# Optimization experiments

Hardware: AMD Instinct MI355X
Metric: run time of the kernel (lower is better)

The kernel has to match this reference:

```python
import jax, jax.numpy as jnp
import numpy as np

N = 131072   # total nodes (4096 molecules x ~32 atoms)
E = 524288   # directed edges (avg degree 4)
G = 4096     # number of graphs
D_IN, D_H, D_OUT = 128, 512, 256
BN_EPS = 1e-5


def setup_inputs() -> dict:
    key = jax.random.key(0)
    ks = jax.random.split(key, 24)
    def rn(i, shape, s=0.05):
        return jax.random.normal(ks[i], shape, jnp.float32) * s
    inp = {
        "x": jax.random.normal(ks[0], (N, D_IN), jnp.float32),
        "edge_index": jax.random.randint(ks[1], (2, E), 0, N),
        "batch": jnp.sort(jax.random.randint(ks[2], (N,), 0, G)),
        # GCN layer weights (stored [in, out]) and biases
        "W1": rn(3, (D_IN, D_H)), "b1": jnp.zeros((D_H,), jnp.float32),
        "W2": rn(4, (D_H, D_H)),  "b2": jnp.zeros((D_H,), jnp.float32),
        "W3": rn(5, (D_H, D_OUT)), "b3": jnp.zeros((D_OUT,), jnp.float32),
        # BatchNorm (eval mode): gamma, beta, running_mean, running_var
        "g1": jnp.ones((D_H,), jnp.float32),  "be1": jnp.zeros((D_H,), jnp.float32),
        "m1": rn(6, (D_H,)),  "v1": jax.random.uniform(ks[7], (D_H,), jnp.float32) + 0.5,
        "g2": jnp.ones((D_H,), jnp.float32),  "be2": jnp.zeros((D_H,), jnp.float32),
        "m2": rn(8, (D_H,)),  "v2": jax.random.uniform(ks[9], (D_H,), jnp.float32) + 0.5,
        "g3": jnp.ones((D_OUT,), jnp.float32), "be3": jnp.zeros((D_OUT,), jnp.float32),
        "m3": rn(10, (D_OUT,)), "v3": jax.random.uniform(ks[11], (D_OUT,), jnp.float32) + 0.5,
        # MLP head
        "Wf1": rn(12, (D_OUT, D_OUT)), "bf1": jnp.zeros((D_OUT,), jnp.float32),
        "Wf2": rn(13, (D_OUT, D_OUT)), "bf2": jnp.zeros((D_OUT,), jnp.float32),
    }
    return inp


def reference(x, edge_index, batch, W1, b1, W2, b2, W3, b3,
              g1, be1, m1, v1, g2, be2, m2, v2, g3, be3, m3, v3,
              Wf1, bf1, Wf2, bf2):
    loop = jnp.arange(N)
    src = jnp.concatenate([edge_index[0], loop])  # add self-loops (PyG GCNConv default)
    dst = jnp.concatenate([edge_index[1], loop])
    deg = jax.ops.segment_sum(jnp.ones((E + N,), x.dtype), dst, num_segments=N)
    dinv = jnp.where(deg > 0, jax.lax.rsqrt(deg), 0.0)
    norm = dinv[src] * dinv[dst]                  # D^{-1/2} A_hat D^{-1/2}

    def gcn(h, W, b):
        h = h @ W                                 # dense GEMM [N, d_out]
        msg = h[src] * norm[:, None]              # gather + scale
        return jax.ops.segment_sum(msg, dst, num_segments=N) + b  # scatter-add

    def bn(h, g, be, m, v):                       # eval-mode BatchNorm1d
        return g * (h - m) * jax.lax.rsqrt(v + BN_EPS) + be

    h = bn(jax.nn.relu(gcn(x, W1, b1)), g1, be1, m1, v1)
    h = bn(jax.nn.relu(gcn(h, W2, b2)), g2, be2, m2, v2)
    h = bn(jax.nn.relu(gcn(h, W3, b3)), g3, be3, m3, v3)

    sums = jax.ops.segment_sum(h, batch, num_segments=G)          # global_mean_pool
    cnt = jax.ops.segment_sum(jnp.ones((N,), h.dtype), batch, num_segments=G)
    pooled = sums / jnp.maximum(cnt, 1.0)[:, None]

    return jax.nn.relu(pooled @ Wf1 + bf1) @ Wf2 + bf2
```

## Files before the change

kernel.cpp:

```cpp
#include <hip/hip_runtime.h>

static constexpr int NN = 131072;
static constexpr int NE = 524288;
static constexpr int NG = 4096;

typedef __attribute__((ext_vector_type(8))) short short8;
typedef __attribute__((ext_vector_type(4))) float f32x4;
typedef __attribute__((ext_vector_type(2))) float f32x2;

__device__ __forceinline__ float bfbits2f(unsigned b) {
    return __uint_as_float(b << 16);
}
__device__ __forceinline__ unsigned short f2bfbits(float f) {
    unsigned u = __float_as_uint(f);
    u += 0x7fffu + ((u >> 16) & 1u);
    return (unsigned short)(u >> 16);
}
__device__ __forceinline__ unsigned pack2(float a, float b) {
    return (unsigned)f2bfbits(a) | ((unsigned)f2bfbits(b) << 16);
}

__device__ __forceinline__ int geti(const void* p, size_t i, int w64) {
    return w64 ? (int)((const long long*)p)[i] : ((const int*)p)[i];
}

#if __has_builtin(__builtin_amdgcn_cvt_pk_f32_fp8) && __has_builtin(__builtin_amdgcn_cvt_pk_fp8_f32)
#define FP8_CVT_HW 1
#else
#define FP8_CVT_HW 0
#endif

__device__ __forceinline__ float e4m32f(unsigned b) {
    unsigned e = (b >> 3) & 0xFu, m = b & 7u;
    float v = e ? __uint_as_float(((e + 120u) << 23) | (m << 20))
                : (float)m * 0.001953125f;
    return (b & 0x80u) ? -v : v;
}
__device__ __forceinline__ unsigned f2e4m3(float f) {
    unsigned u = __float_as_uint(f);
    unsigned s = (u >> 24) & 0x80u;
    unsigned mag = u & 0x7fffffffu;
    if (mag >= 0x43e00000u) return s | 0x7eu;
    if (mag < 0x3c800000u) {
        int q = (int)(__uint_as_float(mag) * 512.0f + 0.5f);
        return s | (unsigned)q;
    }
    unsigned r = mag + 0x0007ffffu + ((mag >> 20) & 1u);
    if (r >= 0x43e00000u) return s | 0x7eu;
    return s | (((r >> 23) - 120u) << 3) | ((r >> 20) & 7u);
}

template<bool HI>
__device__ __forceinline__ unsigned dec_pair(unsigned w) {
#if FP8_CVT_HW
    f32x2 p = __builtin_amdgcn_cvt_pk_f32_fp8((int)w, HI);
    return __builtin_amdgcn_perm(__float_as_uint(p.y), __float_as_uint(p.x), 0x07060302u);
#else
    unsigned b0 = HI ? ((w >> 16) & 255u) : (w & 255u);
    unsigned b1 = HI ? (w >> 24) : ((w >> 8) & 255u);
    return pack2(e4m32f(b0), e4m32f(b1));
#endif
}

__device__ __forceinline__ short8 dec8(uint2 u) {
    union { uint4 q; short8 s; } r;
    r.q.x = dec_pair<false>(u.x);
    r.q.y = dec_pair<true>(u.x);
    r.q.z = dec_pair<false>(u.y);
    r.q.w = dec_pair<true>(u.y);
    return r.s;
}

__device__ __forceinline__ void dec4f(unsigned w, float* v) {
#if FP8_CVT_HW
    f32x2 a = __builtin_amdgcn_cvt_pk_f32_fp8((int)w, false);
    f32x2 b = __builtin_amdgcn_cvt_pk_f32_fp8((int)w, true);
    v[0] = a.x; v[1] = a.y; v[2] = b.x; v[3] = b.y;
#else
#pragma unroll
    for (int i = 0; i < 4; ++i) v[i] = e4m32f((w >> (8 * i)) & 0xffu);
#endif
}

__device__ __forceinline__ unsigned enc4(float a, float b, float c, float d) {
#if FP8_CVT_HW
    int r = __builtin_amdgcn_cvt_pk_fp8_f32(a, b, 0, false);
    r = __builtin_amdgcn_cvt_pk_fp8_f32(c, d, r, true);
    return (unsigned)r;
#else
    return f2e4m3(a) | (f2e4m3(b) << 8) | (f2e4m3(c) << 16) | (f2e4m3(d) << 24);
#endif
}
__device__ __forceinline__ unsigned enc1(float a) {
#if FP8_CVT_HW
    return (unsigned)__builtin_amdgcn_cvt_pk_fp8_f32(a, a, 0, false) & 0xffu;
#else
    return f2e4m3(a);
#endif
}

__device__ __forceinline__ void gld16(const void* g, void* l, int lane) {
#if __has_builtin(__builtin_amdgcn_global_load_lds)
    __builtin_amdgcn_global_load_lds((const __attribute__((address_space(1))) unsigned int*)g,
                                     (__attribute__((address_space(3))) unsigned int*)l, 16, 0, 0);
#else
    *(uint4*)((char*)l + lane * 16) = *(const uint4*)g;
#endif
}

__global__ void k_detect(const void* __restrict__ eidx, const void* __restrict__ batch,
                         int* __restrict__ flags) {
    const int* e32 = (const int*)eidx;
    const int* b32 = (const int*)batch;
    int e64 = (e32[1] == 0 && e32[2001] == 0 && e32[40001] == 0 && e32[2 * NE - 1] == 0) ? 1 : 0;
    int b64 = (b32[NN - 1] == 0) ? 1 : 0;
    flags[0] = e64;
    flags[1] = b64;
}


__global__ void k_zero(int* __restrict__ p, int n) {
    int i = blockIdx.x * 256 + threadIdx.x;
    if (i < n) p[i] = 0;
}

__global__ void k_transpose(const float* __restrict__ W,
                            unsigned short* __restrict__ Wt, int K, int Ncols) {
    int idx = blockIdx.x * 256 + threadIdx.x;
    if (idx >= K * Ncols) return;
    int k = idx / Ncols, n = idx - k * Ncols;
    Wt[n * K + k] = f2bfbits(W[idx]);
}

__global__ void k_bn_prep(const float* __restrict__ g, const float* __restrict__ be,
                          const float* __restrict__ m, const float* __restrict__ v,
                          float* __restrict__ s, float* __restrict__ t, int d) {
    int i = blockIdx.x * 256 + threadIdx.x;
    if (i >= d) return;
    float inv = rsqrtf(v[i] + 1e-5f);
    float sc = g[i] * inv;
    s[i] = sc;
    t[i] = be[i] - m[i] * sc;
}

__global__ void k_deg_count(const void* __restrict__ eidx, const int* __restrict__ flags,
                            int* __restrict__ cnt) {
    int i = blockIdx.x * 256 + threadIdx.x;
    if (i >= NE) return;
    int d = geti(eidx, (size_t)NE + i, flags[0]);
    atomicAdd(&cnt[d], 1);
}

__global__ __launch_bounds__(1024) void k_scan(const int* __restrict__ cnt, int* __restrict__ rowptr,
                                               float* __restrict__ dinv) {
    __shared__ int part[1024];
    const int t = threadIdx.x;
    const int base = t * 128;
    const int4* c4 = (const int4*)(cnt + base);
    int s = 0;
#pragma unroll
    for (int i = 0; i < 32; ++i) { int4 u = c4[i]; s += u.x + u.y + u.z + u.w; }
    part[t] = s;
    __syncthreads();
    for (int off = 1; off < 1024; off <<= 1) {
        int v = (t >= off) ? part[t - off] : 0;
        __syncthreads();
        part[t] += v;
        __syncthreads();
    }
    int ex = (t == 0) ? 0 : part[t - 1];
#pragma unroll
    for (int i = 0; i < 32; ++i) {
        int4 u = c4[i];
        int4 o; o.x = ex; o.y = ex + u.x; o.z = o.y + u.y; o.w = o.z + u.z; ex = o.w + u.w;
        *(int4*)(rowptr + base + 4 * i) = o;
        float4 dv;
        dv.x = rsqrtf((float)(u.x + 1)); dv.y = rsqrtf((float)(u.y + 1));
        dv.z = rsqrtf((float)(u.z + 1)); dv.w = rsqrtf((float)(u.w + 1));
        *(float4*)(dinv + base + 4 * i) = dv;
    }
    if (t == 1023) rowptr[NN] = ex;
}

__global__ void k_fill(const void* __restrict__ eidx, const int* __restrict__ flags,
                       const int* __restrict__ rowptr, int* __restrict__ fillp,
                       int* __restrict__ col) {
    int i = blockIdx.x * 256 + threadIdx.x;
    if (i >= NE) return;
    int e64 = flags[0];
    int s = geti(eidx, (size_t)i, e64);
    int d = geti(eidx, (size_t)NE + i, e64);
    int p = rowptr[d] + atomicAdd(&fillp[d], 1);
    col[p] = s;
}

__global__ void k_gstart(const void* __restrict__ batch, const int* __restrict__ flags,
                         int* __restrict__ gstart) {
    int i = blockIdx.x * 256 + threadIdx.x;
    if (i >= NN) return;
    int b64 = flags[1];
    int b = geti(batch, (size_t)i, b64);
    if (i == 0) {
        for (int g = 0; g <= b; ++g) gstart[g] = 0;
    } else {
        int pb = geti(batch, (size_t)i - 1, b64);
        for (int g = pb + 1; g <= b; ++g) gstart[g] = i;
    }
    if (i == NN - 1) {
        for (int g = b + 1; g <= NG; ++g) gstart[g] = NN;
    }
}

template<int D, int MODE>
__device__ __forceinline__ void load_row_hw(const void* h, int sn, int c0, float* v) {
    if constexpr (MODE == 2) {
        float4 u = *(const float4*)((const float*)h + (size_t)sn * D + c0);
        v[0] = u.x; v[1] = u.y; v[2] = u.z; v[3] = u.w;
    } else {
        uint4 u = *(const uint4*)((const unsigned char*)h + (size_t)sn * D + c0);
        dec4f(u.x, v); dec4f(u.y, v + 4); dec4f(u.z, v + 8); dec4f(u.w, v + 12);
    }
}

template<int D, bool FP8>
__device__ __forceinline__ void store_row_hw(void* out, int n, int c0, const float* v) {
    if constexpr (FP8) {
        uint4 u;
        u.x = enc4(v[0], v[1], v[2], v[3]);
        u.y = enc4(v[4], v[5], v[6], v[7]);
        u.z = enc4(v[8], v[9], v[10], v[11]);
        u.w = enc4(v[12], v[13], v[14], v[15]);
        *(uint4*)((unsigned char*)out + (size_t)n * D + c0) = u;
    } else {
        uint2 u; u.x = pack2(v[0], v[1]); u.y = pack2(v[2], v[3]);
        *(uint2*)((unsigned short*)out + (size_t)n * D + c0) = u;
    }
}

template<int D, int IN_MODE, bool OUT_FP8>
__global__ __launch_bounds__(256) void k_agg_hw(
    const void* __restrict__ h,
    const int* __restrict__ rowptr, const int* __restrict__ col,
    const float* __restrict__ dinv,
    void* __restrict__ out)
{
    constexpr int EPL = (IN_MODE == 1) ? 16 : 4;
    const int n = (blockIdx.x * 256 + threadIdx.x) >> 5;
    const int lane = threadIdx.x & 31;
    const int c0 = lane * EPL;
    float dn = dinv[n];
    float acc[EPL], va[EPL], vb[EPL];

    load_row_hw<D, IN_MODE>(h, n, c0, va);
    float wsl = dn * dn;
#pragma unroll
    for (int i = 0; i < EPL; ++i) acc[i] = va[i] * wsl;

    int e = rowptr[n], e1 = rowptr[n + 1];
    for (; e + 2 <= e1; e += 2) {
        int sa = col[e], sb = col[e + 1];
        float wa = dinv[sa] * dn, wb = dinv[sb] * dn;
        load_row_hw<D, IN_MODE>(h, sa, c0, va);
        load_row_hw<D, IN_MODE>(h, sb, c0, vb);
#pragma unroll
        for (int i = 0; i < EPL; ++i) acc[i] += va[i] * wa + vb[i] * wb;
    }
    if (e < e1) {
        int sa = col[e];
        float wa = dinv[sa] * dn;
        load_row_hw<D, IN_MODE>(h, sa, c0, va);
#pragma unroll
        for (int i = 0; i < EPL; ++i) acc[i] += va[i] * wa;
    }
    store_row_hw<D, OUT_FP8>(out, n, c0, acc);
}

__global__ __launch_bounds__(256) void k_agg_pool(
    const unsigned short* __restrict__ T3,
    const int* __restrict__ rowptr, const int* __restrict__ col,
    const float* __restrict__ dinv,
    const float* __restrict__ b, const float* __restrict__ s, const float* __restrict__ t,
    const int* __restrict__ gstart, unsigned short* __restrict__ pooled)
{
    __shared__ float red[4][256];
    const int g = blockIdx.x;
    const int wave = threadIdx.x >> 6, lane = threadIdx.x & 63;
    const int c0 = lane * 4;
    const int r0 = gstart[g], r1 = gstart[g + 1];
    float p0 = 0, p1 = 0, p2 = 0, p3 = 0;
    const float bc0 = b[c0], bc1 = b[c0 + 1], bc2 = b[c0 + 2], bc3 = b[c0 + 3];
    const float sc0 = s[c0], sc1 = s[c0 + 1], sc2 = s[c0 + 2], sc3 = s[c0 + 3];
    const float tc0 = t[c0], tc1 = t[c0 + 1], tc2 = t[c0 + 2], tc3 = t[c0 + 3];

    for (int n = r0 + wave; n < r1; n += 4) {
        float dn = dinv[n];
        float a0, a1, a2, a3;
        {
            uint2 u = *(const uint2*)(T3 + (size_t)n * 256 + c0);
            float w = dn * dn;
            a0 = bfbits2f(u.x & 0xffffu) * w; a1 = bfbits2f(u.x >> 16) * w;
            a2 = bfbits2f(u.y & 0xffffu) * w; a3 = bfbits2f(u.y >> 16) * w;
        }
        int e = rowptr[n], e1 = rowptr[n + 1];
        for (; e + 2 <= e1; e += 2) {
            int sa = col[e], sb = col[e + 1];
            float wa = dinv[sa] * dn, wb = dinv[sb] * dn;
            uint2 ua = *(const uint2*)(T3 + (size_t)sa * 256 + c0);
            uint2 ub = *(const uint2*)(T3 + (size_t)sb * 256 + c0);
            a0 += bfbits2f(ua.x & 0xffffu) * wa + bfbits2f(ub.x & 0xffffu) * wb;
            a1 += bfbits2f(ua.x >> 16) * wa + bfbits2f(ub.x >> 16) * wb;
            a2 += bfbits2f(ua.y & 0xffffu) * wa + bfbits2f(ub.y & 0xffffu) * wb;
            a3 += bfbits2f(ua.y >> 16) * wa + bfbits2f(ub.y >> 16) * wb;
        }
        if (e < e1) {
            int sa = col[e];
            float wa = dinv[sa] * dn;
            uint2 ua = *(const uint2*)(T3 + (size_t)sa * 256 + c0);
            a0 += bfbits2f(ua.x & 0xffffu) * wa; a1 += bfbits2f(ua.x >> 16) * wa;
            a2 += bfbits2f(ua.y & 0xffffu) * wa; a3 += bfbits2f(ua.y >> 16) * wa;
        }
        p0 += sc0 * fmaxf(a0 + bc0, 0.0f) + tc0;
        p1 += sc1 * fmaxf(a1 + bc1, 0.0f) + tc1;
        p2 += sc2 * fmaxf(a2 + bc2, 0.0f) + tc2;
        p3 += sc3 * fmaxf(a3 + bc3, 0.0f) + tc3;
    }
    red[wave][c0] = p0; red[wave][c0 + 1] = p1; red[wave][c0 + 2] = p2; red[wave][c0 + 3] = p3;
    __syncthreads();
    int ch = threadIdx.x;
    float tot = red[0][ch] + red[1][ch] + red[2][ch] + red[3][ch];
    __syncthreads();
    red[0][ch] = tot;
    __syncthreads();
    if (ch < 128) {
        int ccount = r1 - r0;
        float inv = 1.0f / (float)(ccount > 0 ? ccount : 1);
        pooled[(size_t)g * 256 + 2 * ch] = f2bfbits(red[0][2 * ch] * inv);
        pooled[(size_t)g * 256 + 2 * ch + 1] = f2bfbits(red[0][2 * ch + 1] * inv);
    }
}

template<bool A_FP8, int CB, int OUT_MODE, bool RELU, bool HAS_BN, bool HAS_BIAS>
__global__ __launch_bounds__(256)
void k_gemm(const void* __restrict__ Aptr,
            const unsigned short* __restrict__ Wt,
            const float* __restrict__ bias,
            const float* __restrict__ s, const float* __restrict__ t,
            void* __restrict__ Cptr,
            int K, int Ncols)
{
    __shared__ __align__(16) unsigned short lB[2][2][128 * 32];
    __shared__ __align__(16) unsigned char  lA8[A_FP8 ? 2 : 1][A_FP8 ? 2 : 1][A_FP8 ? 128 * 32 : 16];
    __shared__ __align__(16) unsigned short lA16[A_FP8 ? 1 : 2][A_FP8 ? 1 : 2][A_FP8 ? 8 : 128 * 32];
    const int tid = threadIdx.x;
    const int id = blockIdx.x;
    const int hi = id >> 3;
    const int cblk = hi % CB;
    const int rblk = (hi / CB) * 8 + (id & 7);
    const int bm = rblk * 128;
    const int bn = cblk * 128;
    const int lane = tid & 63;
    const int wave = tid >> 6;
    const int wm = (wave >> 1) * 64;
    const int wn = (wave & 1) * 64;
    const int fr = lane & 15;
    const int fq = lane >> 4;

    f32x4 acc[4][4] = {};
    const int NG64 = K >> 6;

    auto stage = [&](int buf, int k0) {
#pragma unroll
        for (int h = 0; h < 2; ++h) {
            const int kh = k0 + h * 32;
            if constexpr (A_FP8) {
                const unsigned char* g = (const unsigned char*)Aptr
                    + (size_t)(bm + (wave << 5) + (lane >> 1)) * K + kh + (lane & 1) * 16;
                gld16(g, &lA8[buf][h][(wave << 5) * 32], lane);
            } else {
                const unsigned short* Ab = (const unsigned short*)Aptr;
#pragma unroll
                for (int c = 0; c < 2; ++c) {
                    const unsigned short* g = Ab
                        + (size_t)(bm + (wave << 5) + (c << 4) + (lane >> 2)) * K + kh + (lane & 3) * 8;
                    gld16(g, &lA16[buf][h][((wave << 5) + (c << 4)) * 32], lane);
                }
            }
#pragma unroll
            for (int c = 0; c < 2; ++c) {
                const unsigned short* g = Wt
                    + (size_t)(bn + (wave << 5) + (c << 4) + (lane >> 2)) * K + kh + (lane & 3) * 8;
                gld16(g, &lB[buf][h][((wave << 5) + (c << 4)) * 32], lane);
            }
        }
    };

    stage(0, 0);
    __syncthreads();

    int cur = 0;
    for (int kg = 0; kg < NG64; ++kg) {
        if (kg + 1 < NG64) stage(cur ^ 1, (kg + 1) << 6);

#pragma unroll
        for (int h = 0; h < 2; ++h) {
            short8 a[4], b[4];
#pragma unroll
            for (int i = 0; i < 4; ++i) {
                if constexpr (A_FP8)
                    a[i] = dec8(*(const uint2*)&lA8[cur][h][(wm + 16 * i + fr) * 32 + fq * 8]);
                else
                    a[i] = *(const short8*)&lA16[cur][h][(wm + 16 * i + fr) * 32 + fq * 8];
            }
#pragma unroll
            for (int j = 0; j < 4; ++j)
                b[j] = *(const short8*)&lB[cur][h][(wn + 16 * j + fr) * 32 + fq * 8];
#pragma unroll
            for (int i = 0; i < 4; ++i)
#pragma unroll
                for (int j = 0; j < 4; ++j)
                    acc[i][j] = __builtin_amdgcn_mfma_f32_16x16x32_bf16(a[i], b[j], acc[i][j], 0, 0, 0);
        }

        __syncthreads();
        cur ^= 1;
    }

#pragma unroll
    for (int j = 0; j < 4; ++j) {
        int colI = bn + wn + 16 * j + fr;
        float bi = HAS_BIAS ? bias[colI] : 0.0f;
        float sc = HAS_BN ? s[colI] : 1.0f;
        float tc = HAS_BN ? t[colI] : 0.0f;
#pragma unroll
        for (int i = 0; i < 4; ++i) {
#pragma unroll
            for (int r = 0; r < 4; ++r) {
                int row = bm + wm + 16 * i + fq * 4 + r;
                float z = acc[i][j][r] + bi;
                if (RELU) z = fmaxf(z, 0.0f);
                float y = HAS_BN ? (sc * z + tc) : z;
                if constexpr (OUT_MODE == 2)
                    ((float*)Cptr)[(size_t)row * Ncols + colI] = y;
                else if constexpr (OUT_MODE == 1)
                    ((unsigned char*)Cptr)[(size_t)row * Ncols + colI] = (unsigned char)enc1(y);
                else
                    ((unsigned short*)Cptr)[(size_t)row * Ncols + colI] = f2bfbits(y);
            }
        }
    }
}


extern "C" void kernel_launch(void* const* d_in, const int* in_sizes, int n_in,
                              void* d_out, int out_size, void* d_ws, size_t ws_size,
                              hipStream_t stream) {
    const float* x   = (const float*)d_in[0];
    const void* eidx = d_in[1];
    const void* batch = d_in[2];
    const float* W1  = (const float*)d_in[3];
    const float* b1  = (const float*)d_in[4];
    const float* W2  = (const float*)d_in[5];
    const float* b2  = (const float*)d_in[6];
    const float* W3  = (const float*)d_in[7];
    const float* b3  = (const float*)d_in[8];
    const float* g1  = (const float*)d_in[9];
    const float* be1 = (const float*)d_in[10];
    const float* m1  = (const float*)d_in[11];
    const float* v1  = (const float*)d_in[12];
    const float* g2  = (const float*)d_in[13];
    const float* be2 = (const float*)d_in[14];
    const float* m2  = (const float*)d_in[15];
    const float* v2  = (const float*)d_in[16];
    const float* g3  = (const float*)d_in[17];
    const float* be3 = (const float*)d_in[18];
    const float* m3  = (const float*)d_in[19];
    const float* v3  = (const float*)d_in[20];
    const float* Wf1 = (const float*)d_in[21];
    const float* bf1 = (const float*)d_in[22];
    const float* Wf2 = (const float*)d_in[23];
    const float* bf2 = (const float*)d_in[24];

    unsigned char* RB = (unsigned char*)d_ws;
    unsigned char* RA = RB + 67108864;
    unsigned char* EX = RB + 134217728;
    int*   rowptr = (int*)(EX + 0);
    int*   col    = (int*)(EX + 524544);
    float* dinv   = (float*)(EX + 2621696);
    int*   cnt    = (int*)(EX + 3145984);
    int*   fillp  = (int*)(EX + 3670272);
    int*   gstart = (int*)(EX + 4194560);
    float* sbuf   = (float*)(EX + 4211456);
    float *s1 = sbuf, *t1 = sbuf + 512, *s2 = sbuf + 1024, *t2 = sbuf + 1536;
    float *s3 = sbuf + 2048, *t3v = sbuf + 2304;
    unsigned short* Wt1  = (unsigned short*)(EX + 4221696);
    unsigned short* Wt2  = (unsigned short*)(EX + 4352768);
    unsigned short* Wt3  = (unsigned short*)(EX + 4877056);
    unsigned short* Wtf1 = (unsigned short*)(EX + 5139200);
    unsigned short* Wtf2 = (unsigned short*)(EX + 5270272);
    int*   flags = (int*)(EX + 5401344);

    unsigned short* pooled = (unsigned short*)RB;
    unsigned short* z1     = (unsigned short*)(RB + 2097152);

    k_detect<<<1, 1, 0, stream>>>(eidx, batch, flags);
    k_transpose<<<(128 * 512) / 256, 256, 0, stream>>>(W1, Wt1, 128, 512);
    k_transpose<<<(512 * 512) / 256, 256, 0, stream>>>(W2, Wt2, 512, 512);
    k_transpose<<<(512 * 256) / 256, 256, 0, stream>>>(W3, Wt3, 512, 256);
    k_transpose<<<(256 * 256) / 256, 256, 0, stream>>>(Wf1, Wtf1, 256, 256);
    k_transpose<<<(256 * 256) / 256, 256, 0, stream>>>(Wf2, Wtf2, 256, 256);
    k_bn_prep<<<2, 256, 0, stream>>>(g1, be1, m1, v1, s1, t1, 512);
    k_bn_prep<<<2, 256, 0, stream>>>(g2, be2, m2, v2, s2, t2, 512);
    k_bn_prep<<<1, 256, 0, stream>>>(g3, be3, m3, v3, s3, t3v, 256);
    k_zero<<<(2 * NN) / 256, 256, 0, stream>>>(cnt, 2 * NN);
    k_deg_count<<<NE / 256, 256, 0, stream>>>(eidx, flags, cnt);
    k_scan<<<1, 1024, 0, stream>>>(cnt, rowptr, dinv);
    k_fill<<<NE / 256, 256, 0, stream>>>(eidx, flags, rowptr, fillp, col);
    k_gstart<<<NN / 256, 256, 0, stream>>>(batch, flags, gstart);

    const dim3 gagg(NN / 8);

    k_agg_hw<128, 2, false><<<gagg, 256, 0, stream>>>(x, rowptr, col, dinv, RA);
    k_gemm<false, 4, 1, true, true, true><<<4096, 256, 0, stream>>>(RA, Wt1, b1, s1, t1, RB, 128, 512);

    k_agg_hw<512, 1, true><<<gagg, 256, 0, stream>>>(RB, rowptr, col, dinv, RA);
    k_gemm<true, 4, 1, true, true, true><<<4096, 256, 0, stream>>>(RA, Wt2, b2, s2, t2, RB, 512, 512);

    k_gemm<true, 2, 0, false, false, false><<<2048, 256, 0, stream>>>(RB, Wt3, nullptr, nullptr, nullptr, RA, 512, 256);

    k_agg_pool<<<NG, 256, 0, stream>>>((const unsigned short*)RA, rowptr, col, dinv,
                                       b3, s3, t3v, gstart, pooled);

    k_gemm<false, 2, 0, true, false, true><<<64, 256, 0, stream>>>(pooled, Wtf1, bf1, nullptr, nullptr, z1, 256, 256);
    k_gemm<false, 2, 2, false, false, true><<<64, 256, 0, stream>>>(z1, Wtf2, bf2, nullptr, nullptr, d_out, 256, 256);
}
```

Measured before the change: 667.4 us.

## Select intermediate precision tiers by workspace size, keeping bf16 when space allows

```diff
diff --git a/kernel.cpp b/kernel.cpp
--- a/kernel.cpp
+++ b/kernel.cpp
@@ -222,7 +222,7 @@
     }
 }
 
-template<int D, bool FP8>
+template<int D, int EPL, bool FP8>
 __device__ __forceinline__ void store_row_hw(void* out, int n, int c0, const float* v) {
     if constexpr (FP8) {
         uint4 u;
@@ -231,6 +231,15 @@
         u.z = enc4(v[8], v[9], v[10], v[11]);
         u.w = enc4(v[12], v[13], v[14], v[15]);
         *(uint4*)((unsigned char*)out + (size_t)n * D + c0) = u;
+    } else if constexpr (EPL == 16) {
+        unsigned short* p = (unsigned short*)out + (size_t)n * D + c0;
+        uint4 u0, u1;
+        u0.x = pack2(v[0], v[1]);  u0.y = pack2(v[2], v[3]);
+        u0.z = pack2(v[4], v[5]);  u0.w = pack2(v[6], v[7]);
+        u1.x = pack2(v[8], v[9]);  u1.y = pack2(v[10], v[11]);
+        u1.z = pack2(v[12], v[13]); u1.w = pack2(v[14], v[15]);
+        *(uint4*)p = u0;
+        *(uint4*)(p + 8) = u1;
     } else {
         uint2 u; u.x = pack2(v[0], v[1]); u.y = pack2(v[2], v[3]);
         *(uint2*)((unsigned short*)out + (size_t)n * D + c0) = u;
@@ -272,7 +281,7 @@
 #pragma unroll
         for (int i = 0; i < EPL; ++i) acc[i] += va[i] * wa;
     }
-    store_row_hw<D, OUT_FP8>(out, n, c0, acc);
+    store_row_hw<D, EPL, OUT_FP8>(out, n, c0, acc);
 }
 
 __global__ __launch_bounds__(256) void k_agg_pool(
@@ -480,9 +489,26 @@
     const float* Wf2 = (const float*)d_in[23];
     const float* bf2 = (const float*)d_in[24];
 
-    unsigned char* RB = (unsigned char*)d_ws;
-    unsigned char* RA = RB + 67108864;
-    unsigned char* EX = RB + 134217728;
+    constexpr size_t TIER_B_NEED = 201326592ull + 5406720ull;
+    constexpr size_t TIER_A_NEED = 268435456ull + 5406720ull;
+    const int tier = (ws_size >= TIER_A_NEED) ? 0 : (ws_size >= TIER_B_NEED) ? 1 : 2;
+
+    unsigned char* P0;
+    unsigned char* P1;
+    unsigned char* EX;
+    if (tier == 0) {
+        P0 = (unsigned char*)d_ws;
+        P1 = P0 + 134217728;
+        EX = P0 + 268435456;
+    } else if (tier == 1) {
+        P0 = (unsigned char*)d_ws;
+        P1 = P0 + 134217728;
+        EX = P0 + 201326592;
+    } else {
+        P1 = (unsigned char*)d_ws;
+        P0 = P1 + 67108864;
+        EX = P1 + 134217728;
+    }
     int*   rowptr = (int*)(EX + 0);
     int*   col    = (int*)(EX + 524544);
     float* dinv   = (float*)(EX + 2621696);
@@ -499,8 +525,8 @@
     unsigned short* Wtf2 = (unsigned short*)(EX + 5270272);
     int*   flags = (int*)(EX + 5401344);
 
-    unsigned short* pooled = (unsigned short*)RB;
-    unsigned short* z1     = (unsigned short*)(RB + 2097152);
+    unsigned short* pooled = (unsigned short*)P1;
+    unsigned short* z1     = (unsigned short*)(P1 + 2097152);
 
     k_detect<<<1, 1, 0, stream>>>(eidx, batch, flags);
     k_transpose<<<(128 * 512) / 256, 256, 0, stream>>>(W1, Wt1, 128, 512);
@@ -519,15 +545,24 @@
 
     const dim3 gagg(NN / 8);
 
-    k_agg_hw<128, 2, false><<<gagg, 256, 0, stream>>>(x, rowptr, col, dinv, RA);
-    k_gemm<false, 4, 1, true, true, true><<<4096, 256, 0, stream>>>(RA, Wt1, b1, s1, t1, RB, 128, 512);
-
-    k_agg_hw<512, 1, true><<<gagg, 256, 0, stream>>>(RB, rowptr, col, dinv, RA);
-    k_gemm<true, 4, 1, true, true, true><<<4096, 256, 0, stream>>>(RA, Wt2, b2, s2, t2, RB, 512, 512);
-
-    k_gemm<true, 2, 0, false, false, false><<<2048, 256, 0, stream>>>(RB, Wt3, nullptr, nullptr, nullptr, RA, 512, 256);
-
-    k_agg_pool<<<NG, 256, 0, stream>>>((const unsigned short*)RA, rowptr, col, dinv,
+    k_agg_hw<128, 2, false><<<gagg, 256, 0, stream>>>(x, rowptr, col, dinv, P0);
+    k_gemm<false, 4, 1, true, true, true><<<4096, 256, 0, stream>>>(P0, Wt1, b1, s1, t1, P1, 128, 512);
+
+    if (tier == 0) {
+        k_agg_hw<512, 1, false><<<gagg, 256, 0, stream>>>(P1, rowptr, col, dinv, P0);
+        k_gemm<false, 4, 0, true, true, true><<<4096, 256, 0, stream>>>(P0, Wt2, b2, s2, t2, P1, 512, 512);
+        k_gemm<false, 2, 0, false, false, false><<<2048, 256, 0, stream>>>(P1, Wt3, nullptr, nullptr, nullptr, P0, 512, 256);
+    } else if (tier == 1) {
+        k_agg_hw<512, 1, false><<<gagg, 256, 0, stream>>>(P1, rowptr, col, dinv, P0);
+        k_gemm<false, 4, 1, true, true, true><<<4096, 256, 0, stream>>>(P0, Wt2, b2, s2, t2, P1, 512, 512);
+        k_gemm<true, 2, 0, false, false, false><<<2048, 256, 0, stream>>>(P1, Wt3, nullptr, nullptr, nullptr, P0, 512, 256);
+    } else {
+        k_agg_hw<512, 1, true><<<gagg, 256, 0, stream>>>(P1, rowptr, col, dinv, P0);
+        k_gemm<true, 4, 1, true, true, true><<<4096, 256, 0, stream>>>(P0, Wt2, b2, s2, t2, P1, 512, 512);
+        k_gemm<true, 2, 0, false, false, false><<<2048, 256, 0, stream>>>(P1, Wt3, nullptr, nullptr, nullptr, P0, 512, 256);
+    }
+
+    k_agg_pool<<<NG, 256, 0, stream>>>((const unsigned short*)P0, rowptr, col, dinv,
                                        b3, s3, t3v, gstart, pooled);
 
     k_gemm<false, 2, 0, true, false, true><<<64, 256, 0, stream>>>(pooled, Wtf1, bf1, nullptr, nullptr, z1, 256, 256);
```

Measured after the change: 685.8 us. 2.8% more time.
